# Kernel optimization log

Hardware: AMD Instinct MI355X
Metric: run time of the kernel (lower is better)

## Reference

```python
import jax, jax.numpy as jnp
import numpy as np

# ---- static ragged feature layout (from CTGAN metadata) ----
NUM_CLUSTERS = [10, 8, 10, 5, 10, 10, 7, 10, 10, 10]          # per numerical feature
NUM_CATEGORIES = [2, 5, 10, 3, 50, 4, 2, 8, 100, 6, 2, 3, 12, 5, 2, 30, 4, 9, 2, 7]
TAU = 0.2        # GumbelSoftmax temperature (teras default)
BN_EPS = 1e-3    # keras BatchNormalization default epsilon
LATENT_DIM = 128
BATCH = 65536

_seg, _alpha = [], []
_gid = 0
for c in NUM_CLUSTERS:
    _seg.append(_gid); _alpha.append(True); _gid += 1        # alpha scalar (tanh), own segment
    _seg += [_gid] * c; _alpha += [False] * c; _gid += 1     # beta cluster group (gumbel softmax)
for k in NUM_CATEGORIES:
    _seg += [_gid] * k; _alpha += [False] * k; _gid += 1     # categorical group (gumbel softmax)
SEG = jnp.asarray(np.array(_seg, dtype=np.int32))
ALPHA_MASK = jnp.asarray(np.array(_alpha, dtype=bool))
N_SEG = _gid
DATA_DIM = len(_seg)  # 366


def setup_inputs() -> dict:
    key = jax.random.key(0)
    ks = jax.random.split(key, 8)
    z = jax.random.normal(ks[0], (BATCH, LATENT_DIM), dtype=jnp.float32)
    # pre-sampled standard Gumbel noise for the gumbel-softmax groups
    u = jax.random.uniform(ks[1], (BATCH, DATA_DIM), dtype=jnp.float32, minval=1e-6, maxval=1.0 - 1e-6)
    g = -jnp.log(-jnp.log(u))
    def w(k, fi, fo):
        return jax.random.normal(k, (fi, fo), dtype=jnp.float32) * (1.0 / np.sqrt(fi))
    return {
        "z": z, "g": g,
        "W1": w(ks[2], LATENT_DIM, 256), "b1": jnp.zeros((256,), jnp.float32),
        "gamma1": jnp.ones((256,), jnp.float32), "beta1": jnp.zeros((256,), jnp.float32),
        "W2": w(ks[3], LATENT_DIM + 256, 256), "b2": jnp.zeros((256,), jnp.float32),
        "gamma2": jnp.ones((256,), jnp.float32), "beta2": jnp.zeros((256,), jnp.float32),
        "Wout": w(ks[4], LATENT_DIM + 512, DATA_DIM), "bout": jnp.zeros((DATA_DIM,), jnp.float32),
    }


def _bn_relu(h, gamma, beta):
    # training-mode batch norm (batch statistics), as used while training CTGAN
    mu = jnp.mean(h, axis=0)
    var = jnp.var(h, axis=0)
    return jax.nn.relu((h - mu) * jax.lax.rsqrt(var + BN_EPS) * gamma + beta)


def reference(z, g, W1, b1, gamma1, beta1, W2, b2, gamma2, beta2, Wout, bout):
    # CTGAN residual generator layers: out = concat([relu(bn(dense(x))), x])
    h1 = jnp.concatenate([_bn_relu(z @ W1 + b1, gamma1, beta1), z], axis=1)    # [B, 384]
    h2 = jnp.concatenate([_bn_relu(h1 @ W2 + b2, gamma2, beta2), h1], axis=1)  # [B, 640]
    logits = h2 @ Wout + bout                                                  # [B, 366]

    # ragged per-group gumbel-softmax: segment-wise stable softmax over columns
    zt = ((logits + g) / TAU).T                                   # [D, B]
    m = jax.ops.segment_max(zt, SEG, num_segments=N_SEG)          # [S, B]
    e = jnp.exp(zt - m[SEG])
    s = jax.ops.segment_sum(e, SEG, num_segments=N_SEG)
    soft = (e / s[SEG]).T                                         # [B, D]
    # alpha columns: tanh of raw logits; all other columns: group softmax
    return jnp.where(ALPHA_MASK[None, :], jnp.tanh(logits), soft)
```

## Files before the change

### kernel.cpp

```cpp
#include <hip/hip_runtime.h>

typedef _Float16 half_t;
typedef _Float16 half4 __attribute__((ext_vector_type(4)));
typedef _Float16 half8 __attribute__((ext_vector_type(8)));
typedef float f32x4 __attribute__((ext_vector_type(4)));

#define AS1 __attribute__((address_space(1)))
#define AS3 __attribute__((address_space(3)))

static constexpr int NBATCH = 65536;

__global__ __launch_bounds__(256) void k_cvtz(const float* __restrict__ z,
                                              half_t* __restrict__ dst) {
  size_t i = (size_t)blockIdx.x * 256 + threadIdx.x;
  int row = (int)(i >> 4), c8 = (int)(i & 15) << 3;
  const float* s = z + (size_t)row * 128 + c8;
  float4 v0 = *(const float4*)s;
  float4 v1 = *(const float4*)(s + 4);
  half8 h;
  h[0]=(half_t)v0.x; h[1]=(half_t)v0.y; h[2]=(half_t)v0.z; h[3]=(half_t)v0.w;
  h[4]=(half_t)v1.x; h[5]=(half_t)v1.y; h[6]=(half_t)v1.z; h[7]=(half_t)v1.w;
  *(half8*)(dst + (size_t)row * 640 + c8) = h;
}

__global__ __launch_bounds__(256) void k_transpose(const float* __restrict__ W,
                                                   half_t* __restrict__ Wt,
                                                   int K, int N, int total) {
  int i = blockIdx.x * 256 + threadIdx.x;
  if (i >= total) return;
  int n = i / K;
  int k = i - n * K;
  float v = (n < N) ? W[k * N + n] : 0.f;
  Wt[i] = (half_t)v;
}

template<bool STATS, bool F16OUT>
__global__ __launch_bounds__(256) void k_gemm(
    const half_t* __restrict__ A, int lda, int K,
    const half_t* __restrict__ Bt,
    const float* __restrict__ bias,
    half_t* __restrict__ o16, float* __restrict__ o32, int ldo, int ncreal,
    float* __restrict__ ps, float* __restrict__ pq) {
  __shared__ __align__(16) char smem[32768];
  half_t* Asm = (half_t*)smem;
  half_t* Bsm = (half_t*)(smem + 16384);
  const int tid  = threadIdx.x;
  const int lane = tid & 63;
  const int w    = tid >> 6;
  const int wr   = w >> 1, wc = w & 1;
  const int ml   = lane & 15, g = lane >> 4;
  const int brow = blockIdx.x * 128;
  const int bcol = blockIdx.y * 128;
  const int sr  = lane >> 3;
  const int scg = (lane & 7) ^ sr;

  f32x4 acc[4][4];
#pragma unroll
  for (int i = 0; i < 4; i++)
#pragma unroll
    for (int j = 0; j < 4; j++) acc[i][j] = (f32x4){0.f, 0.f, 0.f, 0.f};

  const half_t* Abase = A  + (size_t)brow * lda;
  const half_t* Bbase = Bt + (size_t)bcol * K;

  for (int k0 = 0; k0 < K; k0 += 64) {
    if (k0) __syncthreads();
#pragma unroll
    for (int it = 0; it < 4; it++) {
      int q = it * 4 + w;
      int r = q * 8 + sr;
      const half_t* ga = Abase + (size_t)r * lda + k0 + scg * 8;
      const half_t* gb = Bbase + (size_t)r * K   + k0 + scg * 8;
      __builtin_amdgcn_global_load_lds((AS1 const void*)ga, (AS3 void*)(Asm + q * 512), 16, 0, 0);
      __builtin_amdgcn_global_load_lds((AS1 const void*)gb, (AS3 void*)(Bsm + q * 512), 16, 0, 0);
    }
    __syncthreads();
#pragma unroll
    for (int kk = 0; kk < 64; kk += 16) {
      int k  = kk + g * 4;
      int cs = k >> 3;
      int ko = (k & 7) * 2;
      half4 af[4], bf[4];
#pragma unroll
      for (int fm = 0; fm < 4; fm++) {
        int row = wr * 64 + fm * 16 + ml;
        af[fm] = *(const half4*)((const char*)Asm + row * 128 + ((cs ^ (row & 7)) << 4) + ko);
      }
#pragma unroll
      for (int fn = 0; fn < 4; fn++) {
        int row = wc * 64 + fn * 16 + ml;
        bf[fn] = *(const half4*)((const char*)Bsm + row * 128 + ((cs ^ (row & 7)) << 4) + ko);
      }
#pragma unroll
      for (int fm = 0; fm < 4; fm++)
#pragma unroll
        for (int fn = 0; fn < 4; fn++)
          acc[fm][fn] = __builtin_amdgcn_mfma_f32_16x16x16f16(af[fm], bf[fn], acc[fm][fn], 0, 0, 0);
    }
  }
  __syncthreads();

#pragma unroll
  for (int fn = 0; fn < 4; fn++) {
    int col  = wc * 64 + fn * 16 + ml;
    int gcol = bcol + col;
    float bz = (gcol < ncreal) ? bias[gcol] : 0.f;
    float s = 0.f, q = 0.f;
#pragma unroll
    for (int fm = 0; fm < 4; fm++)
#pragma unroll
      for (int rr = 0; rr < 4; rr++) {
        float v = acc[fm][fn][rr] + bz;
        acc[fm][fn][rr] = v;
        if (STATS) { s += v; q += v * v; }
      }
    if (STATS) {
      s += __shfl_xor(s, 16, 64); s += __shfl_xor(s, 32, 64);
      q += __shfl_xor(q, 16, 64); q += __shfl_xor(q, 32, 64);
      if (g == 0) {
        ps[(size_t)gcol * 1024 + blockIdx.x * 2 + wr] = s;
        pq[(size_t)gcol * 1024 + blockIdx.x * 2 + wr] = q;
      }
    }
  }

  if (F16OUT) {
    half_t* so = (half_t*)smem;
#pragma unroll
    for (int fn = 0; fn < 4; fn++)
#pragma unroll
      for (int fm = 0; fm < 4; fm++)
#pragma unroll
        for (int rr = 0; rr < 4; rr++)
          so[(wr * 64 + fm * 16 + g * 4 + rr) * 128 + wc * 64 + fn * 16 + ml] =
              (half_t)acc[fm][fn][rr];
    __syncthreads();
#pragma unroll
    for (int it = 0; it < 8; it++) {
      int r = it * 16 + (tid >> 4);
      int c = (tid & 15) * 8;
      *(half8*)(o16 + (size_t)(brow + r) * ldo + bcol + c) = *(const half8*)&so[r * 128 + c];
    }
  } else {
    float* so = (float*)smem;
    for (int h = 0; h < 2; h++) {
      if (wr == h) {
#pragma unroll
        for (int fn = 0; fn < 4; fn++)
#pragma unroll
          for (int fm = 0; fm < 4; fm++)
#pragma unroll
            for (int rr = 0; rr < 4; rr++)
              so[(fm * 16 + g * 4 + rr) * 128 + wc * 64 + fn * 16 + ml] = acc[fm][fn][rr];
      }
      __syncthreads();
      int r0 = h * 64;
      for (int i = tid; i < 64 * 64; i += 256) {
        int r  = i >> 6;
        int c2 = (i & 63) * 2;
        int gc = bcol + c2;
        if (gc < ncreal)
          *(float2*)(o32 + (size_t)(brow + r0 + r) * ldo + gc) = *(const float2*)&so[r * 128 + c2];
      }
      __syncthreads();
    }
  }
}

__global__ __launch_bounds__(256) void k_bnfinal(
    const float* __restrict__ ps, const float* __restrict__ pq,
    const float* __restrict__ gamma, const float* __restrict__ beta,
    float* __restrict__ sc, float* __restrict__ sh) {
  int c = blockIdx.x, t = threadIdx.x;
  float s = 0.f, q = 0.f;
#pragma unroll
  for (int i = 0; i < 4; i++) {
    s += ps[(size_t)c * 1024 + t + i * 256];
    q += pq[(size_t)c * 1024 + t + i * 256];
  }
#pragma unroll
  for (int o = 1; o < 64; o <<= 1) { s += __shfl_xor(s, o, 64); q += __shfl_xor(q, o, 64); }
  __shared__ float ss[4], qq[4];
  if ((t & 63) == 0) { ss[t >> 6] = s; qq[t >> 6] = q; }
  __syncthreads();
  if (t == 0) {
    s = ss[0] + ss[1] + ss[2] + ss[3];
    q = qq[0] + qq[1] + qq[2] + qq[3];
    float mu   = s * (1.f / NBATCH);
    float var  = fmaxf(q * (1.f / NBATCH) - mu * mu, 0.f);
    float rstd = rsqrtf(var + 1e-3f);
    float a = gamma[c] * rstd;
    sc[c] = a;
    sh[c] = beta[c] - mu * a;
  }
}

__global__ __launch_bounds__(256) void k_bnrelu(half_t* __restrict__ p,
                                                const float* __restrict__ sc,
                                                const float* __restrict__ sh) {
  size_t i = (size_t)blockIdx.x * 256 + threadIdx.x;
  int row = (int)(i >> 5), c8 = (int)(i & 31) << 3;
  half_t* a = p + (size_t)row * 640 + c8;
  half8 v = *(const half8*)a;
  half8 o;
#pragma unroll
  for (int j = 0; j < 8; j++)
    o[j] = (half_t)fmaxf(fmaf((float)v[j], sc[c8 + j], sh[c8 + j]), 0.f);
  *(half8*)a = o;
}

template<int L>
__device__ __forceinline__ void seg_rt(float* __restrict__ zr, int S) {
  float v[L];
#pragma unroll
  for (int j = 0; j < L; j++) v[j] = zr[S + j];
  float m0 = -1e30f, m1 = -1e30f, m2 = -1e30f, m3 = -1e30f;
#pragma unroll
  for (int j = 0; j < L; j++) {
    if ((j & 3) == 0) m0 = fmaxf(m0, v[j]);
    else if ((j & 3) == 1) m1 = fmaxf(m1, v[j]);
    else if ((j & 3) == 2) m2 = fmaxf(m2, v[j]);
    else m3 = fmaxf(m3, v[j]);
  }
  const float m = fmaxf(fmaxf(m0, m1), fmaxf(m2, m3));
  float s0 = 0.f, s1 = 0.f, s2 = 0.f, s3 = 0.f;
#pragma unroll
  for (int j = 0; j < L; j++) {
    float e = __expf(v[j] - m);
    v[j] = e;
    if ((j & 3) == 0) s0 += e;
    else if ((j & 3) == 1) s1 += e;
    else if ((j & 3) == 2) s2 += e;
    else s3 += e;
  }
  const float inv = 1.0f / ((s0 + s1) + (s2 + s3));
#pragma unroll
  for (int j = 0; j < L; j++) zr[S + j] = v[j] * inv;
}

template<int S, int L>
__device__ __forceinline__ void seg_split(float* __restrict__ zr, int par) {
  constexpr int H = L / 2;
  const int base = S + par * H;
  float v[H];
#pragma unroll
  for (int j = 0; j < H; j++) v[j] = zr[base + j];
  float m0 = -1e30f, m1 = -1e30f, m2 = -1e30f, m3 = -1e30f;
#pragma unroll
  for (int j = 0; j < H; j++) {
    if ((j & 3) == 0) m0 = fmaxf(m0, v[j]);
    else if ((j & 3) == 1) m1 = fmaxf(m1, v[j]);
    else if ((j & 3) == 2) m2 = fmaxf(m2, v[j]);
    else m3 = fmaxf(m3, v[j]);
  }
  float m = fmaxf(fmaxf(m0, m1), fmaxf(m2, m3));
  m = fmaxf(m, __shfl_xor(m, 1, 64));
  float s0 = 0.f, s1 = 0.f, s2 = 0.f, s3 = 0.f;
#pragma unroll
  for (int j = 0; j < H; j++) {
    float e = __expf(v[j] - m);
    v[j] = e;
    if ((j & 3) == 0) s0 += e;
    else if ((j & 3) == 1) s1 += e;
    else if ((j & 3) == 2) s2 += e;
    else s3 += e;
  }
  float s = (s0 + s1) + (s2 + s3);
  s += __shfl_xor(s, 1, 64);
  const float inv = 1.0f / s;
#pragma unroll
  for (int j = 0; j < H; j++) zr[base + j] = v[j] * inv;
}

__device__ __forceinline__ bool is_alpha(int c) {
  const unsigned long long AM0 =
      (1ull << 0) | (1ull << 11) | (1ull << 20) | (1ull << 31) | (1ull << 37) |
      (1ull << 48) | (1ull << 59);
  const unsigned long long AM1 = (1ull << 3) | (1ull << 14) | (1ull << 25);
  if (c >= 90) return false;
  return (((c < 64) ? (AM0 >> c) : (AM1 >> (c - 64))) & 1ull) != 0ull;
}

__global__ __launch_bounds__(512, 2) void k_softmax(const float* __restrict__ g,
                                                    float* __restrict__ out) {
  __shared__ float zb[32][373];
  const int tid = threadIdx.x;
  const size_t base = (size_t)blockIdx.x * 32 * 366;
  for (int i2 = tid; i2 < 32 * 183; i2 += 512) {
    int e0 = i2 * 2;
    int r = e0 / 366;
    int c = e0 - r * 366;
    float2 lg = *(const float2*)(out + base + e0);
    float2 gg = *(const float2*)(g + base + e0);
    zb[r][c]     = is_alpha(c)     ? tanhf(lg.x) : (lg.x + gg.x) * 5.0f;
    zb[r][c + 1] = is_alpha(c + 1) ? tanhf(lg.y) : (lg.y + gg.y) * 5.0f;
  }
  __syncthreads();
  {
    const int lane = tid & 63;
    const int par  = lane & 1;
    float* zr = &zb[lane >> 1][0];
    switch (tid >> 6) {
      case 0: seg_split<184, 100>(zr, par); break;
      case 1: seg_split<120, 50>(zr, par); break;
      case 2: seg_split<314, 30>(zr, par);
              { int sa = par ? 174 : 100; seg_rt<2>(zr, sa); } break;
      case 3: { int sa = par ? 68 : 1;   int sb = par ? 176 : 12;
                seg_rt<10>(zr, sa); seg_rt<8>(zr, sb); } break;
      case 4: { int sa = par ? 79 : 21;  int sb = par ? 359 : 60;
                seg_rt<10>(zr, sa); seg_rt<7>(zr, sb); } break;
      case 5: { int sa = par ? 90 : 38;  int sb = par ? 102 : 32; int sd = par ? 292 : 117;
                seg_rt<10>(zr, sa); seg_rt<5>(zr, sb); seg_rt<3>(zr, sd); } break;
      case 6: { int sa = par ? 107 : 49; int sb = par ? 344 : 170; int sd = par ? 312 : 290;
                seg_rt<10>(zr, sa); seg_rt<4>(zr, sb); seg_rt<2>(zr, sd); } break;
      default:
        if (par == 0) { seg_rt<12>(zr, 295); seg_rt<5>(zr, 307); }
        else          { seg_rt<9>(zr, 348);  seg_rt<6>(zr, 284); seg_rt<2>(zr, 357); }
        break;
    }
  }
  __syncthreads();
  for (int i2 = tid; i2 < 32 * 183; i2 += 512) {
    int e0 = i2 * 2;
    int r = e0 / 366;
    int c = e0 - r * 366;
    float2 o;
    o.x = zb[r][c];
    o.y = zb[r][c + 1];
    *(float2*)(out + base + e0) = o;
  }
}

extern "C" void kernel_launch(void* const* d_in, const int* in_sizes, int n_in,
                              void* d_out, int out_size, void* d_ws, size_t ws_size,
                              hipStream_t stream) {
  const float* z      = (const float*)d_in[0];
  const float* g      = (const float*)d_in[1];
  const float* W1     = (const float*)d_in[2];
  const float* b1     = (const float*)d_in[3];
  const float* gamma1 = (const float*)d_in[4];
  const float* beta1  = (const float*)d_in[5];
  const float* W2     = (const float*)d_in[6];
  const float* b2     = (const float*)d_in[7];
  const float* gamma2 = (const float*)d_in[8];
  const float* beta2  = (const float*)d_in[9];
  const float* Wout   = (const float*)d_in[10];
  const float* bout   = (const float*)d_in[11];
  float* out = (float*)d_out;
  char* ws = (char*)d_ws;

  size_t off = 0;
  half_t* act = (half_t*)(ws + off); off += (size_t)NBATCH * 640 * 2;
  half_t* W1t = (half_t*)(ws + off); off += (size_t)256 * 128 * 2;
  half_t* W2t = (half_t*)(ws + off); off += (size_t)256 * 384 * 2;
  half_t* Wot = (half_t*)(ws + off); off += (size_t)384 * 640 * 2;
  float*  ps  = (float*)(ws + off);  off += (size_t)256 * 1024 * 4;
  float*  pq  = (float*)(ws + off);  off += (size_t)256 * 1024 * 4;
  float*  sc1 = (float*)(ws + off);  off += 256 * 4;
  float*  sh1 = (float*)(ws + off);  off += 256 * 4;
  float*  sc2 = (float*)(ws + off);  off += 256 * 4;
  float*  sh2 = (float*)(ws + off);  off += 256 * 4;
  (void)ws_size; (void)in_sizes; (void)n_in; (void)out_size;

  k_cvtz<<<4096, 256, 0, stream>>>(z, act + 512);
  k_transpose<<<(256 * 128 + 255) / 256, 256, 0, stream>>>(W1, W1t, 128, 256, 256 * 128);
  k_transpose<<<(256 * 384 + 255) / 256, 256, 0, stream>>>(W2, W2t, 384, 256, 256 * 384);
  k_transpose<<<(384 * 640 + 255) / 256, 256, 0, stream>>>(Wout, Wot, 640, 366, 384 * 640);

  k_gemm<true, true><<<dim3(512, 2), 256, 0, stream>>>(
      act + 512, 640, 128, W1t, b1, act + 256, nullptr, 640, 256, ps, pq);
  k_bnfinal<<<256, 256, 0, stream>>>(ps, pq, gamma1, beta1, sc1, sh1);
  k_bnrelu<<<8192, 256, 0, stream>>>(act + 256, sc1, sh1);

  k_gemm<true, true><<<dim3(512, 2), 256, 0, stream>>>(
      act + 256, 640, 384, W2t, b2, act + 0, nullptr, 640, 256, ps, pq);
  k_bnfinal<<<256, 256, 0, stream>>>(ps, pq, gamma2, beta2, sc2, sh2);
  k_bnrelu<<<8192, 256, 0, stream>>>(act + 0, sc2, sh2);

  k_gemm<false, false><<<dim3(512, 3), 256, 0, stream>>>(
      act, 640, 640, Wot, bout, nullptr, out, 366, 366, nullptr, nullptr);

  k_softmax<<<NBATCH / 32, 512, 0, stream>>>(g, out);
}
```

Baseline: 215.4 us.

## Fuse output GEMM with gumbel-softmax epilogue in one kernel

Replaces the third GEMM plus the separate softmax kernel with one kernel. Each 512-thread block computes a 128x384 output tile and runs the tanh and segment-softmax epilogue on it in shared memory, 32 rows at a time. This removes the fp32 logits round trip through global memory and one kernel launch. In exchange it uses 64KB of shared memory, more accumulators per thread and a serialized four-pass epilogue, which may lower occupancy.

```diff
diff --git a/kernel.cpp b/kernel.cpp
--- a/kernel.cpp
+++ b/kernel.cpp
@@ -34,12 +34,11 @@
   Wt[i] = (half_t)v;
 }
 
-template<bool STATS, bool F16OUT>
 __global__ __launch_bounds__(256) void k_gemm(
     const half_t* __restrict__ A, int lda, int K,
     const half_t* __restrict__ Bt,
     const float* __restrict__ bias,
-    half_t* __restrict__ o16, float* __restrict__ o32, int ldo, int ncreal,
+    half_t* __restrict__ o16, int ldo,
     float* __restrict__ ps, float* __restrict__ pq) {
   __shared__ __align__(16) char smem[32768];
   half_t* Asm = (half_t*)smem;
@@ -104,7 +103,7 @@
   for (int fn = 0; fn < 4; fn++) {
     int col  = wc * 64 + fn * 16 + ml;
     int gcol = bcol + col;
-    float bz = (gcol < ncreal) ? bias[gcol] : 0.f;
+    float bz = bias[gcol];
     float s = 0.f, q = 0.f;
 #pragma unroll
     for (int fm = 0; fm < 4; fm++)
@@ -112,58 +111,31 @@
       for (int rr = 0; rr < 4; rr++) {
         float v = acc[fm][fn][rr] + bz;
         acc[fm][fn][rr] = v;
-        if (STATS) { s += v; q += v * v; }
-      }
-    if (STATS) {
-      s += __shfl_xor(s, 16, 64); s += __shfl_xor(s, 32, 64);
-      q += __shfl_xor(q, 16, 64); q += __shfl_xor(q, 32, 64);
-      if (g == 0) {
-        ps[(size_t)gcol * 1024 + blockIdx.x * 2 + wr] = s;
-        pq[(size_t)gcol * 1024 + blockIdx.x * 2 + wr] = q;
-      }
-    }
-  }
-
-  if (F16OUT) {
-    half_t* so = (half_t*)smem;
-#pragma unroll
-    for (int fn = 0; fn < 4; fn++)
-#pragma unroll
-      for (int fm = 0; fm < 4; fm++)
-#pragma unroll
-        for (int rr = 0; rr < 4; rr++)
-          so[(wr * 64 + fm * 16 + g * 4 + rr) * 128 + wc * 64 + fn * 16 + ml] =
-              (half_t)acc[fm][fn][rr];
-    __syncthreads();
-#pragma unroll
-    for (int it = 0; it < 8; it++) {
-      int r = it * 16 + (tid >> 4);
-      int c = (tid & 15) * 8;
-      *(half8*)(o16 + (size_t)(brow + r) * ldo + bcol + c) = *(const half8*)&so[r * 128 + c];
-    }
-  } else {
-    float* so = (float*)smem;
-    for (int h = 0; h < 2; h++) {
-      if (wr == h) {
-#pragma unroll
-        for (int fn = 0; fn < 4; fn++)
-#pragma unroll
-          for (int fm = 0; fm < 4; fm++)
-#pragma unroll
-            for (int rr = 0; rr < 4; rr++)
-              so[(fm * 16 + g * 4 + rr) * 128 + wc * 64 + fn * 16 + ml] = acc[fm][fn][rr];
-      }
-      __syncthreads();
-      int r0 = h * 64;
-      for (int i = tid; i < 64 * 64; i += 256) {
-        int r  = i >> 6;
-        int c2 = (i & 63) * 2;
-        int gc = bcol + c2;
-        if (gc < ncreal)
-          *(float2*)(o32 + (size_t)(brow + r0 + r) * ldo + gc) = *(const float2*)&so[r * 128 + c2];
-      }
-      __syncthreads();
-    }
+        s += v; q += v * v;
+      }
+    s += __shfl_xor(s, 16, 64); s += __shfl_xor(s, 32, 64);
+    q += __shfl_xor(q, 16, 64); q += __shfl_xor(q, 32, 64);
+    if (g == 0) {
+      ps[(size_t)gcol * 1024 + blockIdx.x * 2 + wr] = s;
+      pq[(size_t)gcol * 1024 + blockIdx.x * 2 + wr] = q;
+    }
+  }
+
+  half_t* so = (half_t*)smem;
+#pragma unroll
+  for (int fn = 0; fn < 4; fn++)
+#pragma unroll
+    for (int fm = 0; fm < 4; fm++)
+#pragma unroll
+      for (int rr = 0; rr < 4; rr++)
+        so[(wr * 64 + fm * 16 + g * 4 + rr) * 128 + wc * 64 + fn * 16 + ml] =
+            (half_t)acc[fm][fn][rr];
+  __syncthreads();
+#pragma unroll
+  for (int it = 0; it < 8; it++) {
+    int r = it * 16 + (tid >> 4);
+    int c = (tid & 15) * 8;
+    *(half8*)(o16 + (size_t)(brow + r) * ldo + bcol + c) = *(const half8*)&so[r * 128 + c];
   }
 }
 
@@ -281,53 +253,136 @@
   return (((c < 64) ? (AM0 >> c) : (AM1 >> (c - 64))) & 1ull) != 0ull;
 }
 
-__global__ __launch_bounds__(512, 2) void k_softmax(const float* __restrict__ g,
-                                                    float* __restrict__ out) {
-  __shared__ float zb[32][373];
-  const int tid = threadIdx.x;
-  const size_t base = (size_t)blockIdx.x * 32 * 366;
-  for (int i2 = tid; i2 < 32 * 183; i2 += 512) {
-    int e0 = i2 * 2;
-    int r = e0 / 366;
-    int c = e0 - r * 366;
-    float2 lg = *(const float2*)(out + base + e0);
-    float2 gg = *(const float2*)(g + base + e0);
-    zb[r][c]     = is_alpha(c)     ? tanhf(lg.x) : (lg.x + gg.x) * 5.0f;
-    zb[r][c + 1] = is_alpha(c + 1) ? tanhf(lg.y) : (lg.y + gg.y) * 5.0f;
-  }
-  __syncthreads();
-  {
-    const int lane = tid & 63;
-    const int par  = lane & 1;
-    float* zr = &zb[lane >> 1][0];
-    switch (tid >> 6) {
-      case 0: seg_split<184, 100>(zr, par); break;
-      case 1: seg_split<120, 50>(zr, par); break;
-      case 2: seg_split<314, 30>(zr, par);
-              { int sa = par ? 174 : 100; seg_rt<2>(zr, sa); } break;
-      case 3: { int sa = par ? 68 : 1;   int sb = par ? 176 : 12;
-                seg_rt<10>(zr, sa); seg_rt<8>(zr, sb); } break;
-      case 4: { int sa = par ? 79 : 21;  int sb = par ? 359 : 60;
-                seg_rt<10>(zr, sa); seg_rt<7>(zr, sb); } break;
-      case 5: { int sa = par ? 90 : 38;  int sb = par ? 102 : 32; int sd = par ? 292 : 117;
-                seg_rt<10>(zr, sa); seg_rt<5>(zr, sb); seg_rt<3>(zr, sd); } break;
-      case 6: { int sa = par ? 107 : 49; int sb = par ? 344 : 170; int sd = par ? 312 : 290;
-                seg_rt<10>(zr, sa); seg_rt<4>(zr, sb); seg_rt<2>(zr, sd); } break;
-      default:
-        if (par == 0) { seg_rt<12>(zr, 295); seg_rt<5>(zr, 307); }
-        else          { seg_rt<9>(zr, 348);  seg_rt<6>(zr, 284); seg_rt<2>(zr, 357); }
-        break;
-    }
-  }
-  __syncthreads();
-  for (int i2 = tid; i2 < 32 * 183; i2 += 512) {
-    int e0 = i2 * 2;
-    int r = e0 / 366;
-    int c = e0 - r * 366;
-    float2 o;
-    o.x = zb[r][c];
-    o.y = zb[r][c + 1];
-    *(float2*)(out + base + e0) = o;
+__global__ __launch_bounds__(512, 2) void k_gemm3sm(
+    const half_t* __restrict__ A,
+    const half_t* __restrict__ Bt,
+    const float* __restrict__ bias,
+    const float* __restrict__ gum,
+    float* __restrict__ out) {
+  __shared__ __align__(16) char smem[65536];
+  half_t* Asm = (half_t*)smem;
+  half_t* Bsm = (half_t*)(smem + 16384);
+  float (*zb)[373] = (float(*)[373])smem;
+  const int tid  = threadIdx.x;
+  const int lane = tid & 63;
+  const int w    = tid >> 6;
+  const int wr   = w >> 2;
+  const int wc   = w & 3;
+  const int ml   = lane & 15, g = lane >> 4;
+  const int brow = blockIdx.x * 128;
+  const int sr   = lane >> 3;
+  const int scg  = (lane & 7) ^ sr;
+
+  f32x4 acc[4][6];
+#pragma unroll
+  for (int i = 0; i < 4; i++)
+#pragma unroll
+    for (int j = 0; j < 6; j++) acc[i][j] = (f32x4){0.f, 0.f, 0.f, 0.f};
+
+  const half_t* Abase = A + (size_t)brow * 640;
+
+  for (int k0 = 0; k0 < 640; k0 += 64) {
+    if (k0) __syncthreads();
+#pragma unroll
+    for (int it = 0; it < 2; it++) {
+      int q = it * 8 + w;
+      int r = q * 8 + sr;
+      const half_t* ga = Abase + (size_t)r * 640 + k0 + scg * 8;
+      __builtin_amdgcn_global_load_lds((AS1 const void*)ga, (AS3 void*)(Asm + q * 512), 16, 0, 0);
+    }
+#pragma unroll
+    for (int it = 0; it < 6; it++) {
+      int q = it * 8 + w;
+      int r = q * 8 + sr;
+      const half_t* gb = Bt + (size_t)r * 640 + k0 + scg * 8;
+      __builtin_amdgcn_global_load_lds((AS1 const void*)gb, (AS3 void*)(Bsm + q * 512), 16, 0, 0);
+    }
+    __syncthreads();
+#pragma unroll
+    for (int kk = 0; kk < 64; kk += 16) {
+      int k  = kk + g * 4;
+      int cs = k >> 3;
+      int ko = (k & 7) * 2;
+      half4 af[4], bf[6];
+#pragma unroll
+      for (int fm = 0; fm < 4; fm++) {
+        int row = wr * 64 + fm * 16 + ml;
+        af[fm] = *(const half4*)((const char*)Asm + row * 128 + ((cs ^ (row & 7)) << 4) + ko);
+      }
+#pragma unroll
+      for (int fn = 0; fn < 6; fn++) {
+        int row = wc * 96 + fn * 16 + ml;
+        bf[fn] = *(const half4*)((const char*)Bsm + row * 128 + ((cs ^ (row & 7)) << 4) + ko);
+      }
+#pragma unroll
+      for (int fm = 0; fm < 4; fm++)
+#pragma unroll
+        for (int fn = 0; fn < 6; fn++)
+          acc[fm][fn] = __builtin_amdgcn_mfma_f32_16x16x16f16(af[fm], bf[fn], acc[fm][fn], 0, 0, 0);
+    }
+  }
+
+  for (int b = 0; b < 4; b++) {
+    __syncthreads();
+    if (wr == (b >> 1)) {
+      const int fmb = (b & 1) * 2;
+#pragma unroll
+      for (int fl = 0; fl < 2; fl++) {
+#pragma unroll
+        for (int fn = 0; fn < 6; fn++) {
+          int col = wc * 96 + fn * 16 + ml;
+          if (col < 366) {
+            float bz = bias[col];
+#pragma unroll
+            for (int rr = 0; rr < 4; rr++)
+              zb[fl * 16 + g * 4 + rr][col] = acc[fmb + fl][fn][rr] + bz;
+          }
+        }
+      }
+    }
+    __syncthreads();
+    const size_t gbase = (size_t)(brow + b * 32) * 366;
+    for (int i2 = tid; i2 < 32 * 183; i2 += 512) {
+      int e0 = i2 * 2;
+      int r = e0 / 366;
+      int c = e0 - r * 366;
+      float2 gg = *(const float2*)(gum + gbase + e0);
+      float vx = zb[r][c], vy = zb[r][c + 1];
+      zb[r][c]     = is_alpha(c)     ? tanhf(vx) : (vx + gg.x) * 5.0f;
+      zb[r][c + 1] = is_alpha(c + 1) ? tanhf(vy) : (vy + gg.y) * 5.0f;
+    }
+    __syncthreads();
+    {
+      const int par = lane & 1;
+      float* zr = &zb[lane >> 1][0];
+      switch (w) {
+        case 0: seg_split<184, 100>(zr, par); break;
+        case 1: seg_split<120, 50>(zr, par); break;
+        case 2: seg_split<314, 30>(zr, par);
+                { int sa = par ? 174 : 100; seg_rt<2>(zr, sa); } break;
+        case 3: { int sa = par ? 68 : 1;   int sb = par ? 176 : 12;
+                  seg_rt<10>(zr, sa); seg_rt<8>(zr, sb); } break;
+        case 4: { int sa = par ? 79 : 21;  int sb = par ? 359 : 60;
+                  seg_rt<10>(zr, sa); seg_rt<7>(zr, sb); } break;
+        case 5: { int sa = par ? 90 : 38;  int sb = par ? 102 : 32; int sd = par ? 292 : 117;
+                  seg_rt<10>(zr, sa); seg_rt<5>(zr, sb); seg_rt<3>(zr, sd); } break;
+        case 6: { int sa = par ? 107 : 49; int sb = par ? 344 : 170; int sd = par ? 312 : 290;
+                  seg_rt<10>(zr, sa); seg_rt<4>(zr, sb); seg_rt<2>(zr, sd); } break;
+        default:
+          if (par == 0) { seg_rt<12>(zr, 295); seg_rt<5>(zr, 307); }
+          else          { seg_rt<9>(zr, 348);  seg_rt<6>(zr, 284); seg_rt<2>(zr, 357); }
+          break;
+      }
+    }
+    __syncthreads();
+    for (int i2 = tid; i2 < 32 * 183; i2 += 512) {
+      int e0 = i2 * 2;
+      int r = e0 / 366;
+      float2 o;
+      o.x = zb[r][e0 - r * 366];
+      o.y = zb[r][e0 - r * 366 + 1];
+      *(float2*)(out + gbase + e0) = o;
+    }
   }
 }
 
@@ -367,18 +422,15 @@
   k_transpose<<<(256 * 384 + 255) / 256, 256, 0, stream>>>(W2, W2t, 384, 256, 256 * 384);
   k_transpose<<<(384 * 640 + 255) / 256, 256, 0, stream>>>(Wout, Wot, 640, 366, 384 * 640);
 
-  k_gemm<true, true><<<dim3(512, 2), 256, 0, stream>>>(
-      act + 512, 640, 128, W1t, b1, act + 256, nullptr, 640, 256, ps, pq);
+  k_gemm<<<dim3(512, 2), 256, 0, stream>>>(act + 512, 640, 128, W1t, b1,
+                                           act + 256, 640, ps, pq);
   k_bnfinal<<<256, 256, 0, stream>>>(ps, pq, gamma1, beta1, sc1, sh1);
   k_bnrelu<<<8192, 256, 0, stream>>>(act + 256, sc1, sh1);
 
-  k_gemm<true, true><<<dim3(512, 2), 256, 0, stream>>>(
-      act + 256, 640, 384, W2t, b2, act + 0, nullptr, 640, 256, ps, pq);
+  k_gemm<<<dim3(512, 2), 256, 0, stream>>>(act + 256, 640, 384, W2t, b2,
+                                           act + 0, 640, ps, pq);
   k_bnfinal<<<256, 256, 0, stream>>>(ps, pq, gamma2, beta2, sc2, sh2);
   k_bnrelu<<<8192, 256, 0, stream>>>(act + 0, sc2, sh2);
 
-  k_gemm<false, false><<<dim3(512, 3), 256, 0, stream>>>(
-      act, 640, 640, Wot, bout, nullptr, out, 366, 366, nullptr, nullptr);
-
-  k_softmax<<<NBATCH / 32, 512, 0, stream>>>(g, out);
-}
+  k_gemm3sm<<<512, 512, 0, stream>>>(act, Wot, bout, g, out);
+}
```

New measurement: 392.1 us. 82.1% more time.
